# Performance work log

Measured on AMD Instinct MI355X. Metric: run time of the kernel, lower is better.

## Reference

```python
import jax, jax.numpy as jnp
import numpy as np

B, N, E, C = 1, 100000, 1600000, 128


def setup_inputs() -> dict:
    key = jax.random.key(0)
    k1, k2, k3, k4 = jax.random.split(key, 4)
    x = jax.random.normal(k1, (B, N, C), dtype=jnp.float32)
    edge_index = jax.random.randint(k2, (2, E), 0, N, dtype=jnp.int32)
    W_2 = jax.random.normal(k3, (C,), dtype=jnp.float32)
    W_3 = jax.random.normal(k4, (C,), dtype=jnp.float32)
    return {"x": x, "edge_index": edge_index, "W_2": W_2, "W_3": W_3}


def reference(x, edge_index, W_2, W_3):
    # x: [B, N, C]; edge_index: [2, E] (src, dst)
    src, dst = edge_index[0], edge_index[1]
    num_nodes = x.shape[1]
    # per-edge attention weight: w[b,e] = <(x*W_3)[b,src_e], x[b,dst_e]>
    x3 = (x * W_3)[:, src, :]          # [B, E, C] gather
    x4 = x[:, dst, :]                  # [B, E, C] gather
    w = jnp.einsum('bec,bec->be', x3, x4)  # [B, E]
    # value messages with diagonal W_2 scaling, scattered to destination nodes.
    # Equivalent to out = einsum('bij,bih->bjh', dense_adj(w), x*W_2),
    # where dense_adj[src,dst] = w (to_dense_adj sums duplicate edges; so does segment_sum).
    x2 = x * W_2                       # [B, N, C]
    msg = w[..., None] * x2[:, src, :]  # [B, E, C]
    out = jax.vmap(lambda m: jax.ops.segment_sum(m, dst, num_segments=num_nodes))(msg)
    return out  # [B, N, C]
```

## Files before the change

kernel.cpp:

```cpp
#include <hip/hip_runtime.h>
#include <hip/hip_fp16.h>


#define CCH 128
#define BSHIFT 5
#define BWIDTH 32
#define MAXBIN 4096
#define CH 8192
#define LDSCAP 1280
#define TBINS 16
#define NBLKCAP 256

typedef _Float16 half2_t __attribute__((ext_vector_type(2)));

__device__ __forceinline__ float dot8_f16(const __half2* q, const half2_t* v) {
#if __has_builtin(__builtin_amdgcn_fdot2)
    const half2_t* qv = reinterpret_cast<const half2_t*>(q);
    float p = __builtin_amdgcn_fdot2(qv[0], v[0], 0.f, false);
    p = __builtin_amdgcn_fdot2(qv[1], v[1], p, false);
    p = __builtin_amdgcn_fdot2(qv[2], v[2], p, false);
    p = __builtin_amdgcn_fdot2(qv[3], v[3], p, false);
    return p;
#else
    const __half2* vv = reinterpret_cast<const __half2*>(v);
    __half2 t = __hmul2(q[0], vv[0]);
    t = __hfma2(q[1], vv[1], t);
    t = __hfma2(q[2], vv[2], t);
    t = __hfma2(q[3], vv[3], t);
    float2 tf = __half22float2(t);
    return tf.x + tf.y;
#endif
}


__device__ __forceinline__ void pack_body(const float* __restrict__ x,
                                          __half* __restrict__ xh,
                                          int n4, int i) {
    if (i < n4) {
        float4 v = reinterpret_cast<const float4*>(x)[i];
        __half2* o = reinterpret_cast<__half2*>(xh) + (size_t)i * 2;
        o[0] = __floats2half2_rn(v.x, v.y);
        o[1] = __floats2half2_rn(v.z, v.w);
    }
}


__global__ __launch_bounds__(256) void k_hist_pack(
    const int* __restrict__ dst, int E, int NBIN, int NBLK,
    int* __restrict__ hist_bm,
    const float* __restrict__ x, __half* __restrict__ xh, int n4, int pOff)
{
    __shared__ int cnt[MAXBIN];
    const int tid = threadIdx.x;

    if ((int)blockIdx.x >= NBLK) {
        pack_body(x, xh, n4, (pOff + (int)blockIdx.x - NBLK) * 256 + tid);
        return;
    }

    const int blk = blockIdx.x;
    for (int b = tid; b < NBIN; b += 256) cnt[b] = 0;
    __syncthreads();

    const int e0 = blk * CH;
    #pragma unroll
    for (int k = 0; k < CH / 1024; ++k) {
        const int g = (e0 >> 2) + k * 256 + tid;
        const int e = g << 2;
        if (e >= E) continue;
        if (e + 4 <= E) {
            const int4 d4 = reinterpret_cast<const int4*>(dst)[g];
            atomicAdd(&cnt[d4.x >> BSHIFT], 1);
            atomicAdd(&cnt[d4.y >> BSHIFT], 1);
            atomicAdd(&cnt[d4.z >> BSHIFT], 1);
            atomicAdd(&cnt[d4.w >> BSHIFT], 1);
        } else {
            for (int ee = e; ee < E; ++ee) atomicAdd(&cnt[dst[ee] >> BSHIFT], 1);
        }
    }
    __syncthreads();
    int* hb = hist_bm + (size_t)blk * NBIN;
    for (int b = tid; b < NBIN; b += 256) hb[b] = cnt[b];
}


__global__ __launch_bounds__(256) void k_pscan_pack(
    const int* __restrict__ hist_bm, int NBIN, int NBLK, int nb1,
    int* __restrict__ partial, int* __restrict__ blocksum,
    const float* __restrict__ x, __half* __restrict__ xh, int n4, int pOff)
{
    __shared__ int tile[TBINS][NBLKCAP + 1];
    __shared__ int sdata[256];
    const int t = threadIdx.x;

    if ((int)blockIdx.x >= nb1) {
        pack_body(x, xh, n4, (pOff + (int)blockIdx.x - nb1) * 256 + t);
        return;
    }

    const int B0 = blockIdx.x * TBINS;

    for (int g = t; g < TBINS * (NBLKCAP + 1); g += 256)
        (&tile[0][0])[g] = 0;
    __syncthreads();

    for (int g = t; g < NBLK * TBINS; g += 256) {
        const int blk = g >> 4;
        const int tb  = g & (TBINS - 1);
        const int bin = B0 + tb;
        if (bin < NBIN) tile[tb][blk] = hist_bm[(size_t)blk * NBIN + bin];
    }
    __syncthreads();

    const int tb  = t >> 4;
    const int bk0 = (t & 15) * 16;
    int v[16];
    int local = 0;
    #pragma unroll
    for (int k = 0; k < 16; ++k) { v[k] = tile[tb][bk0 + k]; local += v[k]; }

    sdata[t] = local;
    __syncthreads();
    #pragma unroll
    for (int off = 1; off < 256; off <<= 1) {
        int val = (t >= off) ? sdata[t - off] : 0;
        __syncthreads();
        sdata[t] += val;
        __syncthreads();
    }
    const int incl = sdata[t];
    int run = incl - local;
    if (t == 255) blocksum[blockIdx.x] = incl;

    const int bin = B0 + tb;
    if (bin < NBIN) {
        #pragma unroll
        for (int k = 0; k < 16; ++k) {
            const int blk = bk0 + k;
            if (blk < NBLK) partial[(size_t)bin * NBLK + blk] = run;
            run += v[k];
        }
    }
}


__global__ __launch_bounds__(256) void k_place_pack(
    const int* __restrict__ src, const int* __restrict__ dst, int E,
    int NBIN, int NBLK, int nb1,
    const int* __restrict__ partial, const int* __restrict__ blocksum,
    unsigned int* __restrict__ coarse,
    const float* __restrict__ x, __half* __restrict__ xh, int n4, int pOff)
{
    __shared__ int lcur[MAXBIN];
    __shared__ int sdata[256];
    __shared__ int sblk[256];
    const int tid = threadIdx.x;

    if ((int)blockIdx.x >= NBLK) {
        pack_body(x, xh, n4, (pOff + (int)blockIdx.x - NBLK) * 256 + tid);
        return;
    }

    sdata[tid] = (tid < nb1) ? blocksum[tid] : 0;
    const int own = sdata[tid];
    __syncthreads();
    #pragma unroll
    for (int off = 1; off < 256; off <<= 1) {
        int val = (tid >= off) ? sdata[tid - off] : 0;
        __syncthreads();
        sdata[tid] += val;
        __syncthreads();
    }
    sblk[tid] = sdata[tid] - own;
    __syncthreads();

    const int blk = blockIdx.x;
    for (int b = tid; b < NBIN; b += 256) {
        lcur[b] = partial[(size_t)b * NBLK + blk] + sblk[b / TBINS];
    }
    __syncthreads();

    const int e0 = blk * CH;
    #pragma unroll
    for (int k = 0; k < CH / 1024; ++k) {
        const int g = (e0 >> 2) + k * 256 + tid;
        const int e = g << 2;
        if (e >= E) continue;
        if (e + 4 <= E) {
            const int4 d4 = reinterpret_cast<const int4*>(dst)[g];
            const int4 s4 = reinterpret_cast<const int4*>(src)[g];
            int p;
            p = atomicAdd(&lcur[d4.x >> BSHIFT], 1);
            coarse[p] = (unsigned)s4.x | ((unsigned)(d4.x & (BWIDTH - 1)) << 17);
            p = atomicAdd(&lcur[d4.y >> BSHIFT], 1);
            coarse[p] = (unsigned)s4.y | ((unsigned)(d4.y & (BWIDTH - 1)) << 17);
            p = atomicAdd(&lcur[d4.z >> BSHIFT], 1);
            coarse[p] = (unsigned)s4.z | ((unsigned)(d4.z & (BWIDTH - 1)) << 17);
            p = atomicAdd(&lcur[d4.w >> BSHIFT], 1);
            coarse[p] = (unsigned)s4.w | ((unsigned)(d4.w & (BWIDTH - 1)) << 17);
        } else {
            for (int ee = e; ee < E; ++ee) {
                const int d = dst[ee], s = src[ee];
                int p = atomicAdd(&lcur[d >> BSHIFT], 1);
                coarse[p] = (unsigned)s | ((unsigned)(d & (BWIDTH - 1)) << 17);
            }
        }
    }
}


__global__ __launch_bounds__(256) void k_sort_accum(
    const __half* __restrict__ xh,
    const float* __restrict__ W2,
    const float* __restrict__ W3,
    const unsigned int* __restrict__ coarse,
    const int* __restrict__ partial, const int* __restrict__ blocksum,
    int NBIN, int NBLK, int nb1, int E, int N,
    float* __restrict__ out)
{
    __shared__ unsigned int raw[LDSCAP];
    __shared__ int srcl[LDSCAP];
    __shared__ int cnt[BWIDTH], offs[BWIDTH], cur[BWIDTH];

    const int bin  = blockIdx.x;
    const int tid  = threadIdx.x;
    const int lane = tid & 63;
    const int grp  = lane >> 4;
    const int sl   = lane & 15;
    const int gid  = (tid >> 6) * 4 + grp;
    const int choff = sl << 4;
    const char* xb = (const char*)xh;

    union H { int4 i4; __half2 h[4]; };

    const int node0 = (bin << BSHIFT) + gid * 2;
    const int node1 = node0 + 1;
    H uD0, uD1;
    uD0.i4 = make_int4(0, 0, 0, 0);
    uD1.i4 = make_int4(0, 0, 0, 0);
    if (node0 < N) uD0.i4 = *reinterpret_cast<const int4*>(xb + (((size_t)node0) << 8) + choff);
    if (node1 < N) uD1.i4 = *reinterpret_cast<const int4*>(xb + (((size_t)node1) << 8) + choff);

    const int j1 = bin / TBINS;
    const int j2 = (bin + 1) / TBINS;
    int s = 0;
    #pragma unroll
    for (int k = 0; k < 4; ++k) {
        const int idx = lane + k * 64;
        if (idx < j1) s += blocksum[idx];
    }
    #pragma unroll
    for (int off = 32; off > 0; off >>= 1) s += __shfl_xor(s, off, 64);
    const int pref1 = s;
    const int pref2 = pref1 + ((j2 > j1 && j2 <= nb1) ? blocksum[j1] : 0);

    const size_t i0 = (size_t)bin * NBLK;
    const int beg = partial[i0] + pref1;
    const int end = (bin + 1 < NBIN) ? partial[i0 + NBLK] + pref2 : E;
    const int mtot = end - beg;
    const int m = (mtot < LDSCAP) ? mtot : LDSCAP;

    if (tid < BWIDTH) cnt[tid] = 0;
    __syncthreads();

    for (int i = tid; i < m; i += 256) {
        unsigned u = coarse[beg + i];
        raw[i] = u;
        atomicAdd(&cnt[u >> 17], 1);
    }
    __syncthreads();

    if (tid < BWIDTH) {
        int c = cnt[tid];
        int v = c;
        #pragma unroll
        for (int d2 = 1; d2 < BWIDTH; d2 <<= 1) {
            int t2 = __shfl_up(v, d2, 64);
            if (tid >= d2) v += t2;
        }
        offs[tid] = v - c;
        cur[tid]  = v - c;
    }
    __syncthreads();

    for (int i = tid; i < m; i += 256) {
        const unsigned u = raw[i];
        const int p = atomicAdd(&cur[u >> 17], 1);
        srcl[p] = (int)(u & 0x1FFFFu);
    }
    __syncthreads();

    const float4 w3a = *reinterpret_cast<const float4*>(W3 + sl * 8);
    const float4 w3b = *reinterpret_cast<const float4*>(W3 + sl * 8 + 4);
    const float4 w2a = *reinterpret_cast<const float4*>(W2 + sl * 8);
    const float4 w2b = *reinterpret_cast<const float4*>(W2 + sl * 8 + 4);

    #pragma unroll
    for (int i = 0; i < 2; ++i) {
        const int node = (i == 0) ? node0 : node1;
        if (node >= N) continue;
        const int dl = gid * 2 + i;
        const H uD = (i == 0) ? uD0 : uD1;

        const float2 e0 = __half22float2(uD.h[0]);
        const float2 e1 = __half22float2(uD.h[1]);
        const float2 e2 = __half22float2(uD.h[2]);
        const float2 e3 = __half22float2(uD.h[3]);
        half2_t vh[4];
        {
            __half2 t0 = __floats2half2_rn(w3a.x * e0.x, w3a.y * e0.y);
            __half2 t1 = __floats2half2_rn(w3a.z * e1.x, w3a.w * e1.y);
            __half2 t2 = __floats2half2_rn(w3b.x * e2.x, w3b.y * e2.y);
            __half2 t3 = __floats2half2_rn(w3b.z * e3.x, w3b.w * e3.y);
            vh[0] = *reinterpret_cast<half2_t*>(&t0);
            vh[1] = *reinterpret_cast<half2_t*>(&t1);
            vh[2] = *reinterpret_cast<half2_t*>(&t2);
            vh[3] = *reinterpret_cast<half2_t*>(&t3);
        }

        __half2 acc[4];
        acc[0] = __floats2half2_rn(0.f, 0.f);
        acc[1] = acc[0]; acc[2] = acc[0]; acc[3] = acc[0];

        const int b0 = offs[dl];
        const int c  = cnt[dl];

        int j = 0;
        for (; j + 4 <= c; j += 4) {
            const int s0 = srcl[b0 + j];
            const int s1 = srcl[b0 + j + 1];
            const int s2 = srcl[b0 + j + 2];
            const int s3 = srcl[b0 + j + 3];
            H u0, u1, u2, u3;
            u0.i4 = *reinterpret_cast<const int4*>(xb + (((size_t)s0) << 8) + choff);
            u1.i4 = *reinterpret_cast<const int4*>(xb + (((size_t)s1) << 8) + choff);
            u2.i4 = *reinterpret_cast<const int4*>(xb + (((size_t)s2) << 8) + choff);
            u3.i4 = *reinterpret_cast<const int4*>(xb + (((size_t)s3) << 8) + choff);
            float p0 = dot8_f16(u0.h, vh);
            float p1 = dot8_f16(u1.h, vh);
            float p2 = dot8_f16(u2.h, vh);
            float p3 = dot8_f16(u3.h, vh);
            #pragma unroll
            for (int off = 1; off < 16; off <<= 1) {
                p0 += __shfl_xor(p0, off, 64);
                p1 += __shfl_xor(p1, off, 64);
                p2 += __shfl_xor(p2, off, 64);
                p3 += __shfl_xor(p3, off, 64);
            }
            const __half2 ph0 = __half2half2(__float2half(p0));
            const __half2 ph1 = __half2half2(__float2half(p1));
            const __half2 ph2 = __half2half2(__float2half(p2));
            const __half2 ph3 = __half2half2(__float2half(p3));
            #pragma unroll
            for (int q = 0; q < 4; ++q) {
                acc[q] = __hfma2(ph0, u0.h[q], acc[q]);
                acc[q] = __hfma2(ph1, u1.h[q], acc[q]);
                acc[q] = __hfma2(ph2, u2.h[q], acc[q]);
                acc[q] = __hfma2(ph3, u3.h[q], acc[q]);
            }
        }
        for (; j < c; ++j) {
            H u0;
            u0.i4 = *reinterpret_cast<const int4*>(
                xb + (((size_t)srcl[b0 + j]) << 8) + choff);
            float p = dot8_f16(u0.h, vh);
            #pragma unroll
            for (int off = 1; off < 16; off <<= 1) p += __shfl_xor(p, off, 64);
            const __half2 ph = __half2half2(__float2half(p));
            #pragma unroll
            for (int q = 0; q < 4; ++q) acc[q] = __hfma2(ph, u0.h[q], acc[q]);
        }
        for (int i2 = LDSCAP; i2 < mtot; ++i2) {
            const unsigned u = coarse[beg + i2];
            if ((int)(u >> 17) != dl) continue;
            H u0;
            u0.i4 = *reinterpret_cast<const int4*>(
                xb + (((size_t)(u & 0x1FFFFu)) << 8) + choff);
            float p = dot8_f16(u0.h, vh);
            #pragma unroll
            for (int off = 1; off < 16; off <<= 1) p += __shfl_xor(p, off, 64);
            const __half2 ph = __half2half2(__float2half(p));
            #pragma unroll
            for (int q = 0; q < 4; ++q) acc[q] = __hfma2(ph, u0.h[q], acc[q]);
        }

        const float2 a0 = __half22float2(acc[0]);
        const float2 a1 = __half22float2(acc[1]);
        const float2 a2 = __half22float2(acc[2]);
        const float2 a3 = __half22float2(acc[3]);
        float4 oA = make_float4(a0.x * w2a.x, a0.y * w2a.y, a1.x * w2a.z, a1.y * w2a.w);
        float4 oB = make_float4(a2.x * w2b.x, a2.y * w2b.y, a3.x * w2b.z, a3.y * w2b.w);
        float* orow = out + (size_t)node * CCH + sl * 8;
        *reinterpret_cast<float4*>(orow)     = oA;
        *reinterpret_cast<float4*>(orow + 4) = oB;
    }
}


__global__ __launch_bounds__(256) void edge_gather_scatter(
    const float* __restrict__ x, const int* __restrict__ edge_index,
    const float* __restrict__ W2, const float* __restrict__ W3,
    float* __restrict__ out, int E)
{
    const int e    = (blockIdx.x * blockDim.x + threadIdx.x) >> 6;
    const int lane = threadIdx.x & 63;
    if (e >= E) return;
    const int s = edge_index[e];
    const int d = edge_index[E + e];
    const float2 xs = *reinterpret_cast<const float2*>(x + (size_t)s * CCH + lane * 2);
    const float2 xd = *reinterpret_cast<const float2*>(x + (size_t)d * CCH + lane * 2);
    const float2 w3 = *reinterpret_cast<const float2*>(W3 + lane * 2);
    const float2 w2 = *reinterpret_cast<const float2*>(W2 + lane * 2);
    float p = xs.x * w3.x * xd.x + xs.y * w3.y * xd.y;
    #pragma unroll
    for (int off = 32; off > 0; off >>= 1) p += __shfl_xor(p, off, 64);
    float* o = out + (size_t)d * CCH + lane * 2;
    atomicAdd(o,     p * xs.x * w2.x);
    atomicAdd(o + 1, p * xs.y * w2.y);
}


extern "C" void kernel_launch(void* const* d_in, const int* in_sizes, int n_in,
                              void* d_out, int out_size, void* d_ws, size_t ws_size,
                              hipStream_t stream) {
    const float* x          = (const float*)d_in[0];
    const int*   edge_index = (const int*)  d_in[1];
    const float* W2         = (const float*)d_in[2];
    const float* W3         = (const float*)d_in[3];
    float*       out        = (float*)d_out;

    const int E = in_sizes[1] / 2;
    const int N = out_size / CCH;
    const int* src = edge_index;
    const int* dst = edge_index + E;

    const int NBIN = (N + BWIDTH - 1) >> BSHIFT;
    const int NBLK = (E + CH - 1) / CH;
    const long long Mll = (long long)NBIN * NBLK;
    const int M = (int)Mll;
    const int nb1 = (NBIN + TBINS - 1) / TBINS;

    const size_t xh_bytes = (size_t)N * CCH * 2;
    const size_t need = xh_bytes + (size_t)E * 4 + 2 * (size_t)M * 4 + 1024 * 4;

    const bool aligned16 = (((uintptr_t)src & 15) == 0) && (((uintptr_t)dst & 15) == 0);

    if (N <= (1 << 17) && NBIN <= MAXBIN && NBLK <= NBLKCAP && Mll <= (1LL << 20) &&
        nb1 <= 256 && aligned16 && ws_size >= need) {
        char* base = (char*)d_ws;
        __half* xh       = (__half*)base;        base += xh_bytes;
        unsigned* coarse = (unsigned*)base;      base += (size_t)E * 4;
        int* hist_bm     = (int*)base;           base += (size_t)M * 4;
        int* partial     = (int*)base;           base += (size_t)M * 4;
        int* blocksum    = (int*)base;

        const int n4 = N * CCH / 4;
        const int nPack = (n4 + 255) / 256;
        const int nP1 = (nPack * 35) / 100;
        const int nP2 = (nPack * 40) / 100;
        const int nP3 = nPack - nP1 - nP2;

        k_hist_pack<<<NBLK + nP1, 256, 0, stream>>>(dst, E, NBIN, NBLK, hist_bm,
                                                    x, xh, n4, 0);
        k_pscan_pack<<<nb1 + nP2, 256, 0, stream>>>(hist_bm, NBIN, NBLK, nb1,
                                                    partial, blocksum,
                                                    x, xh, n4, nP1);
        k_place_pack<<<NBLK + nP3, 256, 0, stream>>>(src, dst, E, NBIN, NBLK, nb1,
                                                     partial, blocksum, coarse,
                                                     x, xh, n4, nP1 + nP2);
        k_sort_accum<<<NBIN, 256, 0, stream>>>(xh, W2, W3, coarse,
                                               partial, blocksum,
                                               NBIN, NBLK, nb1, E, N, out);
        return;
    }

    hipMemsetAsync(d_out, 0, (size_t)out_size * sizeof(float), stream);
    const int grid = (E * 64 + 255) / 256;
    edge_gather_scatter<<<grid, 256, 0, stream>>>(x, edge_index, W2, W3, out, E);
}
```

Measured before the change: 119.6 us.

## Fuse histogram, scan and placement into one persistent kernel with grid barriers

Merges the three preprocessing kernels (histogram, partial scan, placement) into one persistent kernel of 512 blocks. Global atomic barriers in workspace replace the kernel boundaries, and a dynamic work counter hands out the fp32-to-fp16 pack work so idle blocks pick it up. This removes two launch gaps and the static pack split between kernels. In exchange it needs a memset of the barrier words, depends on all 512 blocks being co-resident to avoid deadlock, and adds spin-wait latency.

```diff
diff --git a/kernel.cpp b/kernel.cpp
--- a/kernel.cpp
+++ b/kernel.cpp
@@ -10,6 +10,7 @@
 #define LDSCAP 1280
 #define TBINS 16
 #define NBLKCAP 256
+#define NBA 512
 
 typedef _Float16 half2_t __attribute__((ext_vector_type(2)));
 
@@ -32,7 +33,6 @@
 #endif
 }
 
-
 __device__ __forceinline__ void pack_body(const float* __restrict__ x,
                                           __half* __restrict__ xh,
                                           int n4, int i) {
@@ -45,165 +45,173 @@
 }
 
 
-__global__ __launch_bounds__(256) void k_hist_pack(
-    const int* __restrict__ dst, int E, int NBIN, int NBLK,
-    int* __restrict__ hist_bm,
-    const float* __restrict__ x, __half* __restrict__ xh, int n4, int pOff)
-{
-    __shared__ int cnt[MAXBIN];
-    const int tid = threadIdx.x;
-
-    if ((int)blockIdx.x >= NBLK) {
-        pack_body(x, xh, n4, (pOff + (int)blockIdx.x - NBLK) * 256 + tid);
-        return;
-    }
-
-    const int blk = blockIdx.x;
-    for (int b = tid; b < NBIN; b += 256) cnt[b] = 0;
-    __syncthreads();
-
-    const int e0 = blk * CH;
-    #pragma unroll
-    for (int k = 0; k < CH / 1024; ++k) {
-        const int g = (e0 >> 2) + k * 256 + tid;
-        const int e = g << 2;
-        if (e >= E) continue;
-        if (e + 4 <= E) {
-            const int4 d4 = reinterpret_cast<const int4*>(dst)[g];
-            atomicAdd(&cnt[d4.x >> BSHIFT], 1);
-            atomicAdd(&cnt[d4.y >> BSHIFT], 1);
-            atomicAdd(&cnt[d4.z >> BSHIFT], 1);
-            atomicAdd(&cnt[d4.w >> BSHIFT], 1);
-        } else {
-            for (int ee = e; ee < E; ++ee) atomicAdd(&cnt[dst[ee] >> BSHIFT], 1);
-        }
-    }
-    __syncthreads();
-    int* hb = hist_bm + (size_t)blk * NBIN;
-    for (int b = tid; b < NBIN; b += 256) hb[b] = cnt[b];
-}
-
-
-__global__ __launch_bounds__(256) void k_pscan_pack(
-    const int* __restrict__ hist_bm, int NBIN, int NBLK, int nb1,
-    int* __restrict__ partial, int* __restrict__ blocksum,
-    const float* __restrict__ x, __half* __restrict__ xh, int n4, int pOff)
-{
-    __shared__ int tile[TBINS][NBLKCAP + 1];
-    __shared__ int sdata[256];
-    const int t = threadIdx.x;
-
-    if ((int)blockIdx.x >= nb1) {
-        pack_body(x, xh, n4, (pOff + (int)blockIdx.x - nb1) * 256 + t);
-        return;
-    }
-
-    const int B0 = blockIdx.x * TBINS;
-
-    for (int g = t; g < TBINS * (NBLKCAP + 1); g += 256)
-        (&tile[0][0])[g] = 0;
-    __syncthreads();
-
-    for (int g = t; g < NBLK * TBINS; g += 256) {
-        const int blk = g >> 4;
-        const int tb  = g & (TBINS - 1);
-        const int bin = B0 + tb;
-        if (bin < NBIN) tile[tb][blk] = hist_bm[(size_t)blk * NBIN + bin];
-    }
-    __syncthreads();
-
-    const int tb  = t >> 4;
-    const int bk0 = (t & 15) * 16;
-    int v[16];
-    int local = 0;
-    #pragma unroll
-    for (int k = 0; k < 16; ++k) { v[k] = tile[tb][bk0 + k]; local += v[k]; }
-
-    sdata[t] = local;
-    __syncthreads();
-    #pragma unroll
-    for (int off = 1; off < 256; off <<= 1) {
-        int val = (t >= off) ? sdata[t - off] : 0;
-        __syncthreads();
-        sdata[t] += val;
-        __syncthreads();
-    }
-    const int incl = sdata[t];
-    int run = incl - local;
-    if (t == 255) blocksum[blockIdx.x] = incl;
-
-    const int bin = B0 + tb;
-    if (bin < NBIN) {
-        #pragma unroll
-        for (int k = 0; k < 16; ++k) {
-            const int blk = bk0 + k;
-            if (blk < NBLK) partial[(size_t)bin * NBLK + blk] = run;
-            run += v[k];
-        }
-    }
-}
-
-
-__global__ __launch_bounds__(256) void k_place_pack(
+__global__ __launch_bounds__(256, 4) void k_preproc(
+    const float* __restrict__ x, __half* __restrict__ xh, int n4,
     const int* __restrict__ src, const int* __restrict__ dst, int E,
     int NBIN, int NBLK, int nb1,
-    const int* __restrict__ partial, const int* __restrict__ blocksum,
+    int* __restrict__ hist_bm, int* __restrict__ partial, int* __restrict__ blocksum,
     unsigned int* __restrict__ coarse,
-    const float* __restrict__ x, __half* __restrict__ xh, int n4, int pOff)
+    unsigned int* __restrict__ bar, unsigned int* __restrict__ packCur)
 {
-    __shared__ int lcur[MAXBIN];
-    __shared__ int sdata[256];
-    __shared__ int sblk[256];
+    __shared__ int smem[4608];
+    __shared__ unsigned st;
+    const int bid = blockIdx.x;
     const int tid = threadIdx.x;
-
-    if ((int)blockIdx.x >= NBLK) {
-        pack_body(x, xh, n4, (pOff + (int)blockIdx.x - NBLK) * 256 + tid);
-        return;
-    }
-
-    sdata[tid] = (tid < nb1) ? blocksum[tid] : 0;
-    const int own = sdata[tid];
-    __syncthreads();
-    #pragma unroll
-    for (int off = 1; off < 256; off <<= 1) {
-        int val = (tid >= off) ? sdata[tid - off] : 0;
-        __syncthreads();
-        sdata[tid] += val;
-        __syncthreads();
-    }
-    sblk[tid] = sdata[tid] - own;
-    __syncthreads();
-
-    const int blk = blockIdx.x;
-    for (int b = tid; b < NBIN; b += 256) {
-        lcur[b] = partial[(size_t)b * NBLK + blk] + sblk[b / TBINS];
-    }
-    __syncthreads();
-
-    const int e0 = blk * CH;
-    #pragma unroll
-    for (int k = 0; k < CH / 1024; ++k) {
-        const int g = (e0 >> 2) + k * 256 + tid;
-        const int e = g << 2;
-        if (e >= E) continue;
-        if (e + 4 <= E) {
-            const int4 d4 = reinterpret_cast<const int4*>(dst)[g];
-            const int4 s4 = reinterpret_cast<const int4*>(src)[g];
-            int p;
-            p = atomicAdd(&lcur[d4.x >> BSHIFT], 1);
-            coarse[p] = (unsigned)s4.x | ((unsigned)(d4.x & (BWIDTH - 1)) << 17);
-            p = atomicAdd(&lcur[d4.y >> BSHIFT], 1);
-            coarse[p] = (unsigned)s4.y | ((unsigned)(d4.y & (BWIDTH - 1)) << 17);
-            p = atomicAdd(&lcur[d4.z >> BSHIFT], 1);
-            coarse[p] = (unsigned)s4.z | ((unsigned)(d4.z & (BWIDTH - 1)) << 17);
-            p = atomicAdd(&lcur[d4.w >> BSHIFT], 1);
-            coarse[p] = (unsigned)s4.w | ((unsigned)(d4.w & (BWIDTH - 1)) << 17);
-        } else {
-            for (int ee = e; ee < E; ++ee) {
-                const int d = dst[ee], s = src[ee];
-                int p = atomicAdd(&lcur[d >> BSHIFT], 1);
-                coarse[p] = (unsigned)s | ((unsigned)(d & (BWIDTH - 1)) << 17);
-            }
+    const unsigned NBu = gridDim.x;
+    const int T = (n4 + 255) >> 8;
+
+    if (bid < NBLK) {
+        int* cnt = smem;
+        for (int b = tid; b < NBIN; b += 256) cnt[b] = 0;
+        __syncthreads();
+        {
+            const int e0 = bid * CH;
+            #pragma unroll
+            for (int k = 0; k < CH / 1024; ++k) {
+                const int g = (e0 >> 2) + k * 256 + tid;
+                const int e = g << 2;
+                if (e >= E) continue;
+                if (e + 4 <= E) {
+                    const int4 d4 = reinterpret_cast<const int4*>(dst)[g];
+                    atomicAdd(&cnt[d4.x >> BSHIFT], 1);
+                    atomicAdd(&cnt[d4.y >> BSHIFT], 1);
+                    atomicAdd(&cnt[d4.z >> BSHIFT], 1);
+                    atomicAdd(&cnt[d4.w >> BSHIFT], 1);
+                } else {
+                    for (int ee = e; ee < E; ++ee) atomicAdd(&cnt[dst[ee] >> BSHIFT], 1);
+                }
+            }
+        }
+        __syncthreads();
+        {
+            int* hb = hist_bm + (size_t)bid * NBIN;
+            for (int b = tid; b < NBIN; b += 256) hb[b] = cnt[b];
+        }
+        __syncthreads();
+        if (tid == 0)
+            __hip_atomic_fetch_add(&bar[0], 1u, __ATOMIC_RELEASE, __HIP_MEMORY_SCOPE_AGENT);
+
+        if (bid < nb1) {
+            if (tid == 0)
+                while (__hip_atomic_load(&bar[0], __ATOMIC_ACQUIRE, __HIP_MEMORY_SCOPE_AGENT) < NBu)
+                    __builtin_amdgcn_s_sleep(8);
+            __syncthreads();
+
+            int (*tile)[NBLKCAP + 1] = reinterpret_cast<int(*)[NBLKCAP + 1]>(smem);
+            int* sdt = smem + TBINS * (NBLKCAP + 1);
+            const int B0 = bid * TBINS;
+            for (int g = tid; g < TBINS * (NBLKCAP + 1); g += 256)
+                (&tile[0][0])[g] = 0;
+            __syncthreads();
+            for (int g = tid; g < NBLK * TBINS; g += 256) {
+                const int blk = g >> 4;
+                const int tb  = g & (TBINS - 1);
+                const int bin = B0 + tb;
+                if (bin < NBIN) tile[tb][blk] = hist_bm[(size_t)blk * NBIN + bin];
+            }
+            __syncthreads();
+            const int tb  = tid >> 4;
+            const int bk0 = (tid & 15) * 16;
+            int v[16];
+            int local = 0;
+            #pragma unroll
+            for (int k = 0; k < 16; ++k) { v[k] = tile[tb][bk0 + k]; local += v[k]; }
+            sdt[tid] = local;
+            __syncthreads();
+            #pragma unroll
+            for (int off = 1; off < 256; off <<= 1) {
+                int val = (tid >= off) ? sdt[tid - off] : 0;
+                __syncthreads();
+                sdt[tid] += val;
+                __syncthreads();
+            }
+            const int incl = sdt[tid];
+            int run = incl - local;
+            if (tid == 255) blocksum[bid] = incl;
+            const int bin = B0 + tb;
+            if (bin < NBIN) {
+                #pragma unroll
+                for (int k = 0; k < 16; ++k) {
+                    const int blk = bk0 + k;
+                    if (blk < NBLK) partial[(size_t)bin * NBLK + blk] = run;
+                    run += v[k];
+                }
+            }
+        }
+        __syncthreads();
+        if (tid == 0)
+            __hip_atomic_fetch_add(&bar[1], 1u, __ATOMIC_RELEASE, __HIP_MEMORY_SCOPE_AGENT);
+        if (tid == 0)
+            while (__hip_atomic_load(&bar[1], __ATOMIC_ACQUIRE, __HIP_MEMORY_SCOPE_AGENT) < NBu)
+                __builtin_amdgcn_s_sleep(8);
+        __syncthreads();
+
+        {
+            int* lcur = smem;
+            int* sd   = smem + MAXBIN;
+            int* sb   = smem + MAXBIN + 256;
+            sd[tid] = (tid < nb1) ? blocksum[tid] : 0;
+            const int own = sd[tid];
+            __syncthreads();
+            #pragma unroll
+            for (int off = 1; off < 256; off <<= 1) {
+                int val = (tid >= off) ? sd[tid - off] : 0;
+                __syncthreads();
+                sd[tid] += val;
+                __syncthreads();
+            }
+            sb[tid] = sd[tid] - own;
+            __syncthreads();
+
+            for (int b = tid; b < NBIN; b += 256)
+                lcur[b] = partial[(size_t)b * NBLK + bid] + sb[b / TBINS];
+            __syncthreads();
+
+            const int e0 = bid * CH;
+            #pragma unroll
+            for (int k = 0; k < CH / 1024; ++k) {
+                const int g = (e0 >> 2) + k * 256 + tid;
+                const int e = g << 2;
+                if (e >= E) continue;
+                if (e + 4 <= E) {
+                    const int4 d4 = reinterpret_cast<const int4*>(dst)[g];
+                    const int4 s4 = reinterpret_cast<const int4*>(src)[g];
+                    int p;
+                    p = atomicAdd(&lcur[d4.x >> BSHIFT], 1);
+                    coarse[p] = (unsigned)s4.x | ((unsigned)(d4.x & (BWIDTH - 1)) << 17);
+                    p = atomicAdd(&lcur[d4.y >> BSHIFT], 1);
+                    coarse[p] = (unsigned)s4.y | ((unsigned)(d4.y & (BWIDTH - 1)) << 17);
+                    p = atomicAdd(&lcur[d4.z >> BSHIFT], 1);
+                    coarse[p] = (unsigned)s4.z | ((unsigned)(d4.z & (BWIDTH - 1)) << 17);
+                    p = atomicAdd(&lcur[d4.w >> BSHIFT], 1);
+                    coarse[p] = (unsigned)s4.w | ((unsigned)(d4.w & (BWIDTH - 1)) << 17);
+                } else {
+                    for (int ee = e; ee < E; ++ee) {
+                        const int d = dst[ee], s = src[ee];
+                        int p = atomicAdd(&lcur[d >> BSHIFT], 1);
+                        coarse[p] = (unsigned)s | ((unsigned)(d & (BWIDTH - 1)) << 17);
+                    }
+                }
+            }
+        }
+    } else {
+        __syncthreads();
+        if (tid == 0) {
+            __hip_atomic_fetch_add(&bar[0], 1u, __ATOMIC_RELEASE, __HIP_MEMORY_SCOPE_AGENT);
+            __hip_atomic_fetch_add(&bar[1], 1u, __ATOMIC_RELEASE, __HIP_MEMORY_SCOPE_AGENT);
+        }
+    }
+
+    for (;;) {
+        __syncthreads();
+        if (tid == 0) st = atomicAdd(packCur, 8u);
+        __syncthreads();
+        const unsigned t0 = st;
+        if (t0 >= (unsigned)T) break;
+        #pragma unroll
+        for (int k = 0; k < 8; ++k) {
+            const unsigned t = t0 + k;
+            if (t < (unsigned)T) pack_body(x, xh, n4, (int)t * 256 + tid);
         }
     }
 }
@@ -441,33 +449,28 @@
     const int nb1 = (NBIN + TBINS - 1) / TBINS;
 
     const size_t xh_bytes = (size_t)N * CCH * 2;
-    const size_t need = xh_bytes + (size_t)E * 4 + 2 * (size_t)M * 4 + 1024 * 4;
+    const size_t need = xh_bytes + (size_t)E * 4 + 2 * (size_t)M * 4 + 1024 * 4 + 64;
 
     const bool aligned16 = (((uintptr_t)src & 15) == 0) && (((uintptr_t)dst & 15) == 0);
 
     if (N <= (1 << 17) && NBIN <= MAXBIN && NBLK <= NBLKCAP && Mll <= (1LL << 20) &&
-        nb1 <= 256 && aligned16 && ws_size >= need) {
+        nb1 <= 256 && NBLK < NBA && nb1 < NBA && aligned16 && ws_size >= need) {
         char* base = (char*)d_ws;
-        __half* xh       = (__half*)base;        base += xh_bytes;
-        unsigned* coarse = (unsigned*)base;      base += (size_t)E * 4;
-        int* hist_bm     = (int*)base;           base += (size_t)M * 4;
-        int* partial     = (int*)base;           base += (size_t)M * 4;
-        int* blocksum    = (int*)base;
+        __half* xh        = (__half*)base;       base += xh_bytes;
+        unsigned* coarse  = (unsigned*)base;     base += (size_t)E * 4;
+        int* hist_bm      = (int*)base;          base += (size_t)M * 4;
+        int* partial      = (int*)base;          base += (size_t)M * 4;
+        int* blocksum     = (int*)base;          base += 1024 * 4;
+        unsigned* bar     = (unsigned*)base;
+        unsigned* packCur = bar + 2;
 
         const int n4 = N * CCH / 4;
-        const int nPack = (n4 + 255) / 256;
-        const int nP1 = (nPack * 35) / 100;
-        const int nP2 = (nPack * 40) / 100;
-        const int nP3 = nPack - nP1 - nP2;
-
-        k_hist_pack<<<NBLK + nP1, 256, 0, stream>>>(dst, E, NBIN, NBLK, hist_bm,
-                                                    x, xh, n4, 0);
-        k_pscan_pack<<<nb1 + nP2, 256, 0, stream>>>(hist_bm, NBIN, NBLK, nb1,
-                                                    partial, blocksum,
-                                                    x, xh, n4, nP1);
-        k_place_pack<<<NBLK + nP3, 256, 0, stream>>>(src, dst, E, NBIN, NBLK, nb1,
-                                                     partial, blocksum, coarse,
-                                                     x, xh, n4, nP1 + nP2);
+
+        hipMemsetAsync(bar, 0, 16, stream);
+        k_preproc<<<NBA, 256, 0, stream>>>(x, xh, n4, src, dst, E,
+                                           NBIN, NBLK, nb1,
+                                           hist_bm, partial, blocksum, coarse,
+                                           bar, packCur);
         k_sort_accum<<<NBIN, 256, 0, stream>>>(xh, W2, W3, coarse,
                                                partial, blocksum,
                                                NBIN, NBLK, nb1, E, N, out);
```

Measured after the change: 204.6 us. 1.71x slower.
